# Kernel tuning notes

Measured on AMD Instinct MI355X. Metric: run time of the kernel, lower is better.

The kernel has to match this reference:

```python
import jax, jax.numpy as jnp
import numpy as np

N_NODES = 200000
N_EDGES = 640000
IN_DIM, H1, H2, OUT_DIM = 128, 64, 32, 20


def _glorot(key, shape):
    fan_in, fan_out = shape[0], shape[1]
    lim = float(np.sqrt(6.0 / (fan_in + fan_out)))
    return jax.random.uniform(key, shape, jnp.float32, -lim, lim)


def setup_inputs() -> dict:
    key = jax.random.key(0)
    ks = jax.random.split(key, 8)
    x = jax.random.normal(ks[0], (N_NODES, IN_DIM), jnp.float32)
    edge_index = jax.random.randint(ks[1], (2, N_EDGES), 0, N_NODES, jnp.int64)
    # SAGEConv params: lin_l (neighbor path, with bias), lin_r (root path, no bias)
    return {
        "x": x,
        "edge_index": edge_index,
        "Wl1": _glorot(ks[2], (IN_DIM, H1)), "bl1": jnp.zeros((H1,), jnp.float32),
        "Wr1": _glorot(ks[3], (IN_DIM, H1)),
        "Wl2": _glorot(ks[4], (H1, H2)), "bl2": jnp.zeros((H2,), jnp.float32),
        "Wr2": _glorot(ks[5], (H1, H2)),
        "Wl3": _glorot(ks[6], (H2, OUT_DIM)), "bl3": jnp.zeros((OUT_DIM,), jnp.float32),
        "Wr3": _glorot(ks[7], (H2, OUT_DIM)),
    }


def _sage_conv(x, src, dst, inv_deg, Wl, bl, Wr):
    # mean-aggregate neighbor features: scatter-add x[src] into dst, divide by in-degree
    msgs = x[src]                                            # [E, D] gather
    agg = jax.ops.segment_sum(msgs, dst, num_segments=N_NODES)  # [N, D]
    agg = agg * inv_deg[:, None]                             # mean
    return agg @ Wl + bl + x @ Wr                            # lin_l(agg) + lin_r(x)


def reference(x, edge_index, Wl1, bl1, Wr1, Wl2, bl2, Wr2, Wl3, bl3, Wr3):
    src, dst = edge_index[0], edge_index[1]
    deg = jax.ops.segment_sum(jnp.ones((src.shape[0],), x.dtype), dst,
                              num_segments=N_NODES)
    inv_deg = jnp.where(deg > 0, 1.0 / jnp.maximum(deg, 1.0), 0.0)

    h = jax.nn.relu(_sage_conv(x, src, dst, inv_deg, Wl1, bl1, Wr1))
    # dropout layers are identity in eval mode
    h = jax.nn.relu(_sage_conv(h, src, dst, inv_deg, Wl2, bl2, Wr2))
    return _sage_conv(h, src, dst, inv_deg, Wl3, bl3, Wr3)
```

## Files before the change

### kernel.cpp

```cpp
#include <hip/hip_runtime.h>
#include <hip/hip_bf16.h>


typedef __attribute__((ext_vector_type(8))) short short8;
typedef __attribute__((ext_vector_type(4))) float f32x4;

__device__ inline unsigned short f2b(float x) {
    return __bfloat16_as_ushort(__float2bfloat16(x));
}
__device__ inline float b2f(unsigned short u) {
    return __uint_as_float(((unsigned)u) << 16);
}

__device__ __forceinline__ void gload_lds16(const void* g, void* l) {
    __builtin_amdgcn_global_load_lds(
        (const __attribute__((address_space(1))) void*)g,
        (__attribute__((address_space(3))) void*)l, 16, 0, 0);
}


__global__ void zero_ints(int* __restrict__ p, int n) {
    int i = blockIdx.x * blockDim.x + threadIdx.x;
    if (i < n) p[i] = 0;
}

__global__ void hist_kernel(const int* __restrict__ dst, int* __restrict__ deg, int E) {
    int i = blockIdx.x * blockDim.x + threadIdx.x;
    if (i < E) atomicAdd(&deg[dst[i]], 1);
}

__global__ void scan_reduce(const int* __restrict__ deg, int* __restrict__ bsum, int n) {
    __shared__ int s[256];
    int i = blockIdx.x * 256 + threadIdx.x;
    s[threadIdx.x] = (i < n) ? deg[i] : 0;
    __syncthreads();
    for (int off = 128; off > 0; off >>= 1) {
        if (threadIdx.x < off) s[threadIdx.x] += s[threadIdx.x + off];
        __syncthreads();
    }
    if (threadIdx.x == 0) bsum[blockIdx.x] = s[0];
}

__global__ void scan_top(int* __restrict__ bsum, int nb) {
    __shared__ int s[1024];
    int t = threadIdx.x;
    int v = (t < nb) ? bsum[t] : 0;
    s[t] = v;
    __syncthreads();
    for (int off = 1; off < 1024; off <<= 1) {
        int add = (t >= off) ? s[t - off] : 0;
        __syncthreads();
        s[t] += add;
        __syncthreads();
    }
    if (t < nb) bsum[t] = s[t] - v;
}

__global__ void scan_final(const int* __restrict__ deg, const int* __restrict__ bsum,
                           int* __restrict__ rowptr, int* __restrict__ cursor,
                           int n, int E) {
    __shared__ int s[256];
    int t = threadIdx.x;
    int i = blockIdx.x * 256 + t;
    int v = (i < n) ? deg[i] : 0;
    s[t] = v;
    __syncthreads();
    for (int off = 1; off < 256; off <<= 1) {
        int add = (t >= off) ? s[t - off] : 0;
        __syncthreads();
        s[t] += add;
        __syncthreads();
    }
    int excl = s[t] - v + bsum[blockIdx.x];
    if (i < n) {
        rowptr[i] = excl;
        cursor[i] = excl;
    }
    if (i == 0) rowptr[n] = E;
}

__global__ void fill_kernel(const int* __restrict__ src, const int* __restrict__ dst,
                            int* __restrict__ cursor, int* __restrict__ csr, int E) {
    int e = blockIdx.x * blockDim.x + threadIdx.x;
    if (e < E) {
        int pos = atomicAdd(&cursor[dst[e]], 1);
        csr[pos] = src[e];
    }
}


__launch_bounds__(256, 2)
__global__ void proj1_mfma(const float* __restrict__ x,
                           const float* __restrict__ Wl,
                           const float* __restrict__ Wr,
                           const float* __restrict__ bl,
                           unsigned short* __restrict__ pv,
                           unsigned short* __restrict__ rv,
                           int n) {
    constexpr int S = 4;
    constexpr int TWB = 4;
    constexpr int NCH = TWB * S * 64;

    __shared__ unsigned short sW[NCH * 8];
    __shared__ float sX[2][64 * 128];

    const int b = (int)blockIdx.x;
    const int ch = (b >> 3) & 1;
    const int blk = (b & 7) | ((b >> 4) << 3);
    const int nblk = (int)gridDim.x >> 1;

    const int tid = threadIdx.x;
    for (int chunk = tid; chunk < NCH; chunk += 256) {
        const int lane_c = chunk & 63;
        const int rest = chunk >> 6;
        const int s = rest % S;
        const int t = rest / S;
        const int c = (ch * TWB + t) * 16 + (lane_c & 15);
        const int k0 = s * 32 + (lane_c >> 4) * 8;
        short8 pack;
#pragma unroll
        for (int j = 0; j < 8; ++j) {
            const int k = k0 + j;
            float w = (c < 64) ? Wl[k * 64 + c] : Wr[k * 64 + (c - 64)];
            pack[j] = (short)f2b(w);
        }
        *reinterpret_cast<short8*>(&sW[(size_t)chunk * 8]) = pack;
    }

    const int wave = tid >> 6, lane = tid & 63;
    const int rg = wave;
    const int q = lane >> 4, ln = lane & 15;

    int colg[4];
    float bias[4];
#pragma unroll
    for (int t = 0; t < 4; ++t) {
        colg[t] = ch * 64 + t * 16 + ln;
        bias[t] = (colg[t] >= 64) ? bl[colg[t] - 64] : 0.0f;
    }

    auto stage = [&](int d, int nb) {
#pragma unroll
        for (int i = 0; i < 8; ++i) {
            const int cbase = wave * 512 + i * 64;
            const int ci = cbase + lane;
            const int rl = ci >> 5;
            const int cc = ci & 31;
            int row = nb + rl;
            if (row >= n) row = n - 1;
            const float* g = x + (size_t)row * 128 + (size_t)((cc ^ (rl & 7)) << 2);
            char* l = (char*)&sX[d][0] + (size_t)cbase * 16;
            gload_lds16(g, l);
        }
    };

    auto compute = [&](int d, int nb) {
        const int rowb = nb + rg * 16;
        const int rl = rg * 16 + ln;
        const int swz = rl & 7;
        const float* xbase = &sX[d][(size_t)rl * 128];
        f32x4 acc[4];
#pragma unroll
        for (int t = 0; t < 4; ++t) acc[t] = (f32x4){0.f, 0.f, 0.f, 0.f};
#pragma unroll
        for (int s = 0; s < S; ++s) {
            const int c0 = s * 8 + q * 2;
            float4 v0 = *reinterpret_cast<const float4*>(xbase + ((c0 ^ swz) << 2));
            float4 v1 = *reinterpret_cast<const float4*>(xbase + (((c0 + 1) ^ swz) << 2));
            short8 a;
            a[0] = (short)f2b(v0.x); a[1] = (short)f2b(v0.y);
            a[2] = (short)f2b(v0.z); a[3] = (short)f2b(v0.w);
            a[4] = (short)f2b(v1.x); a[5] = (short)f2b(v1.y);
            a[6] = (short)f2b(v1.z); a[7] = (short)f2b(v1.w);
#pragma unroll
            for (int t = 0; t < 4; ++t) {
                short8 bf = *reinterpret_cast<const short8*>(
                    &sW[((size_t)(t * S + s)) * 512 + (size_t)lane * 8]);
                acc[t] = __builtin_amdgcn_mfma_f32_16x16x32_bf16(a, bf, acc[t], 0, 0, 0);
            }
        }
#pragma unroll
        for (int t = 0; t < 4; ++t) {
            const int c = colg[t];
#pragma unroll
            for (int rr = 0; rr < 4; ++rr) {
                const int row = rowb + q * 4 + rr;
                if (row < n) {
                    if (c < 64)
                        pv[(size_t)row * 64 + c] = f2b(acc[t][rr]);
                    else
                        rv[(size_t)row * 64 + (c - 64)] = f2b(acc[t][rr] + bias[t]);
                }
            }
        }
    };

    constexpr int npi = 64;
    const int stride = nblk * npi;
    int nb = blk * npi;
    if (nb >= n) return;
    stage(0, nb);
    __syncthreads();
    while (true) {
        const int nb1 = nb + stride;
        if (nb1 < n) stage(1, nb1);
        compute(0, nb);
        __syncthreads();
        if (nb1 >= n) break;
        const int nb2 = nb1 + stride;
        if (nb2 < n) stage(0, nb2);
        compute(1, nb1);
        __syncthreads();
        nb = nb2;
        if (nb >= n) break;
    }
}


template <int DIN, int DP, int DR, int DT2, int CH, int NU,
          bool RELU, bool IN_BF16, bool OUT_BF16>
__launch_bounds__(256, 4)
__global__ void proj_mfma(const void* __restrict__ xv,
                          const float* __restrict__ Wl,
                          const float* __restrict__ Wr,
                          const float* __restrict__ bl,
                          void* __restrict__ pv,
                          void* __restrict__ rv,
                          int n) {
    constexpr int WAVES = 4;
    constexpr int TILES = DT2 / 16;
    constexpr int TW = TILES / CH;
    constexpr int S = DIN / 32;
    constexpr int NCH = TW * S * 64;

    __shared__ unsigned short sF[NCH * 8];

    const int ch   = (CH > 1) ? ((int)blockIdx.x % CH) : 0;
    const int blk  = (int)blockIdx.x / CH;
    const int nblk = (int)gridDim.x / CH;

    const int tid = threadIdx.x;
    for (int chunk = tid; chunk < NCH; chunk += 256) {
        const int lane_c = chunk & 63;
        const int rest = chunk >> 6;
        const int s = rest % S;
        const int t = rest / S;
        const int c = (ch * TW + t) * 16 + (lane_c & 15);
        const int k0 = s * 32 + (lane_c >> 4) * 8;
        short8 pack;
#pragma unroll
        for (int j = 0; j < 8; ++j) {
            float w = 0.f;
            const int k = k0 + j;
            if (c < DP) w = Wl[k * DP + c];
            else if (c < DP + DR) w = Wr[k * DR + (c - DP)];
            pack[j] = (short)f2b(w);
        }
        *reinterpret_cast<short8*>(&sF[(size_t)chunk * 8]) = pack;
    }
    __syncthreads();

    const int wave = tid >> 6, lane = tid & 63;
    const int ng = wave;
    const int q = lane >> 4, ln = lane & 15;
    const int colbase = ch * (TW * 16);

    const unsigned short* fbase = &sF[(size_t)lane * 8];

    int colg[TW];
    float bias[TW];
#pragma unroll
    for (int t = 0; t < TW; ++t) {
        colg[t] = colbase + t * 16 + ln;
        bias[t] = (colg[t] >= DP && colg[t] < DP + DR) ? bl[colg[t] - DP] : 0.0f;
    }

    float4 rf0[NU][2 * S], rf1[NU][2 * S];
    short8 rb0[NU][S], rb1[NU][S];

    auto load_groups = [&](float4 (&rf)[NU][2 * S], short8 (&rb)[NU][S], int nbase) {
#pragma unroll
        for (int g = 0; g < NU; ++g) {
            const int base = nbase + (ng * NU + g) * 16;
            if (base >= n) continue;
            if constexpr (IN_BF16) {
                const unsigned short* xr =
                    (const unsigned short*)xv + (size_t)(base + ln) * DIN + q * 8;
#pragma unroll
                for (int s = 0; s < S; ++s)
                    rb[g][s] = *reinterpret_cast<const short8*>(xr + s * 32);
            } else {
                const float* xr = (const float*)xv + (size_t)(base + ln) * DIN + q * 8;
#pragma unroll
                for (int s = 0; s < S; ++s) {
                    rf[g][2 * s]     = *reinterpret_cast<const float4*>(xr + s * 32);
                    rf[g][2 * s + 1] = *reinterpret_cast<const float4*>(xr + s * 32 + 4);
                }
            }
        }
    };

    auto compute_groups = [&](float4 (&rf)[NU][2 * S], short8 (&rb)[NU][S], int nbase) {
#pragma unroll
        for (int g = 0; g < NU; ++g) {
            const int base = nbase + (ng * NU + g) * 16;
            if (base >= n) continue;
            short8 af[S];
#pragma unroll
            for (int s = 0; s < S; ++s) {
                if constexpr (IN_BF16) {
                    short8 a = rb[g][s];
                    if (RELU) {
#pragma unroll
                        for (int j = 0; j < 8; ++j)
                            a[j] = ((short)a[j] < 0) ? (short)0 : a[j];
                    }
                    af[s] = a;
                } else {
                    float4 v0 = rf[g][2 * s], v1 = rf[g][2 * s + 1];
                    if (RELU) {
                        v0.x = fmaxf(v0.x, 0.0f); v0.y = fmaxf(v0.y, 0.0f);
                        v0.z = fmaxf(v0.z, 0.0f); v0.w = fmaxf(v0.w, 0.0f);
                        v1.x = fmaxf(v1.x, 0.0f); v1.y = fmaxf(v1.y, 0.0f);
                        v1.z = fmaxf(v1.z, 0.0f); v1.w = fmaxf(v1.w, 0.0f);
                    }
                    short8 a;
                    a[0] = (short)f2b(v0.x); a[1] = (short)f2b(v0.y);
                    a[2] = (short)f2b(v0.z); a[3] = (short)f2b(v0.w);
                    a[4] = (short)f2b(v1.x); a[5] = (short)f2b(v1.y);
                    a[6] = (short)f2b(v1.z); a[7] = (short)f2b(v1.w);
                    af[s] = a;
                }
            }

            f32x4 acc[TW];
#pragma unroll
            for (int t = 0; t < TW; ++t) acc[t] = (f32x4){0.f, 0.f, 0.f, 0.f};
#pragma unroll
            for (int s = 0; s < S; ++s)
#pragma unroll
                for (int t = 0; t < TW; ++t) {
                    short8 bf = *reinterpret_cast<const short8*>(
                        fbase + (size_t)(t * S + s) * 512);
                    acc[t] = __builtin_amdgcn_mfma_f32_16x16x32_bf16(
                        af[s], bf, acc[t], 0, 0, 0);
                }

#pragma unroll
            for (int t = 0; t < TW; ++t) {
                const int c = colg[t];
#pragma unroll
                for (int rr = 0; rr < 4; ++rr) {
                    const int row = base + q * 4 + rr;
                    if (c < DP) {
                        if constexpr (OUT_BF16)
                            ((unsigned short*)pv)[(size_t)row * DP + c] = f2b(acc[t][rr]);
                        else
                            ((float*)pv)[(size_t)row * DP + c] = acc[t][rr];
                    } else if (c < DP + DR) {
                        const float v = acc[t][rr] + bias[t];
                        if constexpr (OUT_BF16)
                            ((unsigned short*)rv)[(size_t)row * DR + (c - DP)] = f2b(v);
                        else
                            ((float*)rv)[(size_t)row * DR + (c - DP)] = v;
                    }
                }
            }
        }
    };

    const int npi = WAVES * NU * 16;
    const int stride = nblk * npi;
    int nb = blk * npi;
    if (nb >= n) return;
    load_groups(rf0, rb0, nb);
    while (true) {
        const int nb1 = nb + stride;
        if (nb1 < n) load_groups(rf1, rb1, nb1);
        compute_groups(rf0, rb0, nb);
        nb = nb1;
        if (nb >= n) break;
        const int nb2 = nb + stride;
        if (nb2 < n) load_groups(rf0, rb0, nb2);
        compute_groups(rf1, rb1, nb);
        nb = nb2;
        if (nb >= n) break;
    }
}


template <int D, int L>
__global__ void agg_bf16(const int* __restrict__ rowptr,
                         const int* __restrict__ csr,
                         const unsigned short* __restrict__ p,
                         unsigned short* __restrict__ out,
                         int n) {
    constexpr int RQ = D / 8;
    long long gid = (long long)blockIdx.x * blockDim.x + threadIdx.x;
    int d = (int)(gid / L);
    int l = (int)(gid % L);
    if (d >= n) return;
    int beg = rowptr[d], end = rowptr[d + 1];
    int deg = end - beg;
    if (deg <= 0) return;

    const short8* pr = reinterpret_cast<const short8*>(p);
    float s[8];
#pragma unroll
    for (int j = 0; j < 8; ++j) s[j] = 0.0f;

    int i = beg;
    for (; i + 4 <= end; i += 4) {
        int e0 = csr[i], e1 = csr[i + 1], e2 = csr[i + 2], e3 = csr[i + 3];
        short8 a = pr[(size_t)e0 * RQ + l];
        short8 b = pr[(size_t)e1 * RQ + l];
        short8 c = pr[(size_t)e2 * RQ + l];
        short8 e = pr[(size_t)e3 * RQ + l];
#pragma unroll
        for (int j = 0; j < 8; ++j)
            s[j] += (b2f((unsigned short)a[j]) + b2f((unsigned short)b[j])) +
                    (b2f((unsigned short)c[j]) + b2f((unsigned short)e[j]));
    }
    for (; i < end; ++i) {
        short8 a = pr[(size_t)csr[i] * RQ + l];
#pragma unroll
        for (int j = 0; j < 8; ++j) s[j] += b2f((unsigned short)a[j]);
    }

    const float inv = 1.0f / (float)deg;
    short8* o = reinterpret_cast<short8*>(out) + (size_t)d * RQ + l;
    short8 cur = *o;
#pragma unroll
    for (int j = 0; j < 8; ++j) {
        float v = b2f((unsigned short)cur[j]) + s[j] * inv;
        cur[j] = (short)f2b(v);
    }
    *o = cur;
}

template <int D, int L>
__global__ void agg_f32(const int* __restrict__ rowptr,
                        const int* __restrict__ csr,
                        const float* __restrict__ p,
                        float* __restrict__ out,
                        int n) {
    constexpr int RQ = D / 4;
    static_assert(L == RQ, "agg_f32: one float4 per lane");
    long long gid = (long long)blockIdx.x * blockDim.x + threadIdx.x;
    int d = (int)(gid / L);
    int l = (int)(gid % L);
    if (d >= n) return;
    int beg = rowptr[d], end = rowptr[d + 1];
    int deg = end - beg;
    if (deg <= 0) return;

    const float4* pr = reinterpret_cast<const float4*>(p);
    float sx = 0.f, sy = 0.f, sz = 0.f, sw = 0.f;
    int i = beg;
    for (; i + 4 <= end; i += 4) {
        int s0 = csr[i], s1 = csr[i + 1], s2 = csr[i + 2], s3 = csr[i + 3];
        float4 a = pr[(size_t)s0 * RQ + l];
        float4 b = pr[(size_t)s1 * RQ + l];
        float4 c = pr[(size_t)s2 * RQ + l];
        float4 e = pr[(size_t)s3 * RQ + l];
        sx += (a.x + b.x) + (c.x + e.x);
        sy += (a.y + b.y) + (c.y + e.y);
        sz += (a.z + b.z) + (c.z + e.z);
        sw += (a.w + b.w) + (c.w + e.w);
    }
    for (; i < end; ++i) {
        float4 a = pr[(size_t)csr[i] * RQ + l];
        sx += a.x; sy += a.y; sz += a.z; sw += a.w;
    }
    const float inv = 1.0f / (float)deg;
    float4* o = reinterpret_cast<float4*>(out) + (size_t)d * RQ + l;
    float4 cur = *o;
    cur.x += sx * inv; cur.y += sy * inv;
    cur.z += sz * inv; cur.w += sw * inv;
    *o = cur;
}


extern "C" void kernel_launch(void* const* d_in, const int* in_sizes, int n_in,
                              void* d_out, int out_size, void* d_ws, size_t ws_size,
                              hipStream_t stream) {
    const float* x   = (const float*)d_in[0];
    const int*   ei  = (const int*)d_in[1];
    const float* Wl1 = (const float*)d_in[2];
    const float* bl1 = (const float*)d_in[3];
    const float* Wr1 = (const float*)d_in[4];
    const float* Wl2 = (const float*)d_in[5];
    const float* bl2 = (const float*)d_in[6];
    const float* Wr2 = (const float*)d_in[7];
    const float* Wl3 = (const float*)d_in[8];
    const float* bl3 = (const float*)d_in[9];
    const float* Wr3 = (const float*)d_in[10];
    float* out = (float*)d_out;

    const int N = in_sizes[0] / 128;
    const int E = in_sizes[1] / 2;
    const int* src  = ei;
    const int* dstp = ei + E;

    unsigned short* A1 = (unsigned short*)d_ws;
    unsigned short* Bb = A1 + (size_t)N * 64;
    unsigned short* A2 = Bb + (size_t)N * 64;
    unsigned short* Cb = A2 + (size_t)N * 32;
    float* A3 = (float*)(Cb + (size_t)N * 32);
    int* rowptr = (int*)(A3 + (size_t)N * 20);
    int* csr    = rowptr + (N + 1);

    int* degi   = (int*)A3;
    int* cursor = degi + N;
    int* bsum   = cursor + N;

    const int NB = (N + 255) / 256;

    zero_ints<<<NB, 256, 0, stream>>>(degi, N);
    hist_kernel<<<(E + 255) / 256, 256, 0, stream>>>(dstp, degi, E);
    scan_reduce<<<NB, 256, 0, stream>>>(degi, bsum, N);
    scan_top<<<1, 1024, 0, stream>>>(bsum, NB);
    scan_final<<<NB, 256, 0, stream>>>(degi, bsum, rowptr, cursor, N, E);
    fill_kernel<<<(E + 255) / 256, 256, 0, stream>>>(src, dstp, cursor, csr, E);

    proj1_mfma<<<512, 256, 0, stream>>>(x, Wl1, Wr1, bl1, A1, Bb, N);
    agg_bf16<64, 8><<<(int)(((long long)N * 8 + 255) / 256), 256, 0, stream>>>(
        rowptr, csr, A1, Bb, N);

    proj_mfma<64, 32, 32, 64, 1, 2, true, true, true><<<1563, 256, 0, stream>>>(
        Bb, Wl2, Wr2, bl2, A2, Cb, N);
    agg_bf16<32, 4><<<(int)(((long long)N * 4 + 255) / 256), 256, 0, stream>>>(
        rowptr, csr, A2, Cb, N);

    proj_mfma<32, 20, 20, 48, 1, 2, true, true, false><<<1563, 256, 0, stream>>>(
        Cb, Wl3, Wr3, bl3, A3, out, N);
    agg_f32<20, 5><<<(int)(((long long)N * 5 + 255) / 256), 256, 0, stream>>>(
        rowptr, csr, A3, out, N);
}
```

Before: 335.7 us.

## Stage layer-2/3 projection inputs through LDS with async global-to-LDS double buffering

Replaces the register-prefetched proj_mfma for layers 2 and 3 with proj_lds. The new kernel copies 64-row bf16 input tiles into XOR-swizzled shared memory using global_load_lds, double-buffered across grid-stride iterations, before the MFMA reads them. The grid shrinks to 1024 blocks, and the zero-fill kernel becomes hipMemsetAsync. The intent is more coalesced loads and overlap of memory with compute, at the cost of extra barriers and more LDS use per block. The first weight-staging loop has no barrier after it, which relies on the later __syncthreads before compute.

```diff
diff --git a/kernel.cpp b/kernel.cpp
--- a/kernel.cpp
+++ b/kernel.cpp
@@ -18,11 +18,6 @@
         (__attribute__((address_space(3))) void*)l, 16, 0, 0);
 }
 
-
-__global__ void zero_ints(int* __restrict__ p, int n) {
-    int i = blockIdx.x * blockDim.x + threadIdx.x;
-    if (i < n) p[i] = 0;
-}
 
 __global__ void hist_kernel(const int* __restrict__ dst, int* __restrict__ deg, int E) {
     int i = blockIdx.x * blockDim.x + threadIdx.x;
@@ -101,8 +96,8 @@
     constexpr int TWB = 4;
     constexpr int NCH = TWB * S * 64;
 
-    __shared__ unsigned short sW[NCH * 8];
-    __shared__ float sX[2][64 * 128];
+    __shared__ __attribute__((aligned(16))) unsigned short sW[NCH * 8];
+    __shared__ __attribute__((aligned(16))) float sX[2][64 * 128];
 
     const int b = (int)blockIdx.x;
     const int ch = (b >> 3) & 1;
@@ -217,35 +212,33 @@
 }
 
 
-template <int DIN, int DP, int DR, int DT2, int CH, int NU,
-          bool RELU, bool IN_BF16, bool OUT_BF16>
+template <int DIN, int DP, int DR, int DT2, bool RELU, bool OUT_BF16>
 __launch_bounds__(256, 4)
-__global__ void proj_mfma(const void* __restrict__ xv,
-                          const float* __restrict__ Wl,
-                          const float* __restrict__ Wr,
-                          const float* __restrict__ bl,
-                          void* __restrict__ pv,
-                          void* __restrict__ rv,
-                          int n) {
-    constexpr int WAVES = 4;
+__global__ void proj_lds(const unsigned short* __restrict__ xv,
+                         const float* __restrict__ Wl,
+                         const float* __restrict__ Wr,
+                         const float* __restrict__ bl,
+                         void* __restrict__ pv,
+                         void* __restrict__ rv,
+                         int n) {
+    constexpr int S = DIN / 32;
     constexpr int TILES = DT2 / 16;
-    constexpr int TW = TILES / CH;
-    constexpr int S = DIN / 32;
-    constexpr int NCH = TW * S * 64;
-
-    __shared__ unsigned short sF[NCH * 8];
-
-    const int ch   = (CH > 1) ? ((int)blockIdx.x % CH) : 0;
-    const int blk  = (int)blockIdx.x / CH;
-    const int nblk = (int)gridDim.x / CH;
-
+    constexpr int CR = DIN / 8;
+    constexpr int NCH = TILES * S * 64;
+
+    __shared__ __attribute__((aligned(16))) unsigned short sW[NCH * 8];
+    __shared__ __attribute__((aligned(16))) unsigned short sX[2][64 * DIN];
+
+    const int blk = (int)blockIdx.x;
+    const int nblk = (int)gridDim.x;
     const int tid = threadIdx.x;
+
     for (int chunk = tid; chunk < NCH; chunk += 256) {
         const int lane_c = chunk & 63;
         const int rest = chunk >> 6;
         const int s = rest % S;
         const int t = rest / S;
-        const int c = (ch * TW + t) * 16 + (lane_c & 15);
+        const int c = t * 16 + (lane_c & 15);
         const int k0 = s * 32 + (lane_c >> 4) * 8;
         short8 pack;
 #pragma unroll
@@ -256,102 +249,68 @@
             else if (c < DP + DR) w = Wr[k * DR + (c - DP)];
             pack[j] = (short)f2b(w);
         }
-        *reinterpret_cast<short8*>(&sF[(size_t)chunk * 8]) = pack;
-    }
-    __syncthreads();
+        *reinterpret_cast<short8*>(&sW[(size_t)chunk * 8]) = pack;
+    }
 
     const int wave = tid >> 6, lane = tid & 63;
-    const int ng = wave;
+    const int rg = wave;
     const int q = lane >> 4, ln = lane & 15;
-    const int colbase = ch * (TW * 16);
-
-    const unsigned short* fbase = &sF[(size_t)lane * 8];
-
-    int colg[TW];
-    float bias[TW];
-#pragma unroll
-    for (int t = 0; t < TW; ++t) {
-        colg[t] = colbase + t * 16 + ln;
+
+    int colg[TILES];
+    float bias[TILES];
+#pragma unroll
+    for (int t = 0; t < TILES; ++t) {
+        colg[t] = t * 16 + ln;
         bias[t] = (colg[t] >= DP && colg[t] < DP + DR) ? bl[colg[t] - DP] : 0.0f;
     }
 
-    float4 rf0[NU][2 * S], rf1[NU][2 * S];
-    short8 rb0[NU][S], rb1[NU][S];
-
-    auto load_groups = [&](float4 (&rf)[NU][2 * S], short8 (&rb)[NU][S], int nbase) {
-#pragma unroll
-        for (int g = 0; g < NU; ++g) {
-            const int base = nbase + (ng * NU + g) * 16;
-            if (base >= n) continue;
-            if constexpr (IN_BF16) {
-                const unsigned short* xr =
-                    (const unsigned short*)xv + (size_t)(base + ln) * DIN + q * 8;
-#pragma unroll
-                for (int s = 0; s < S; ++s)
-                    rb[g][s] = *reinterpret_cast<const short8*>(xr + s * 32);
-            } else {
-                const float* xr = (const float*)xv + (size_t)(base + ln) * DIN + q * 8;
-#pragma unroll
-                for (int s = 0; s < S; ++s) {
-                    rf[g][2 * s]     = *reinterpret_cast<const float4*>(xr + s * 32);
-                    rf[g][2 * s + 1] = *reinterpret_cast<const float4*>(xr + s * 32 + 4);
-                }
+    auto stage = [&](int d, int nb) {
+#pragma unroll
+        for (int i = 0; i < CR / 4; ++i) {
+            const int cbase = wave * (16 * CR) + i * 64;
+            const int ci = cbase + lane;
+            const int rl = ci / CR;
+            const int cc = ci & (CR - 1);
+            int row = nb + rl;
+            if (row >= n) row = n - 1;
+            const unsigned short* g =
+                xv + (size_t)row * DIN + (size_t)((cc ^ (rl & (CR - 1))) << 3);
+            char* l = (char*)&sX[d][0] + (size_t)cbase * 16;
+            gload_lds16(g, l);
+        }
+    };
+
+    auto compute = [&](int d, int nb) {
+        const int rl = rg * 16 + ln;
+        const int swz = rl & (CR - 1);
+        const unsigned short* rowb = &sX[d][(size_t)rl * DIN];
+        f32x4 acc[TILES];
+#pragma unroll
+        for (int t = 0; t < TILES; ++t) acc[t] = (f32x4){0.f, 0.f, 0.f, 0.f};
+#pragma unroll
+        for (int s = 0; s < S; ++s) {
+            const int c0 = s * 4 + q;
+            short8 a = *reinterpret_cast<const short8*>(rowb + (size_t)((c0 ^ swz) << 3));
+            if (RELU) {
+#pragma unroll
+                for (int j = 0; j < 8; ++j)
+                    a[j] = ((short)a[j] < 0) ? (short)0 : a[j];
             }
-        }
-    };
-
-    auto compute_groups = [&](float4 (&rf)[NU][2 * S], short8 (&rb)[NU][S], int nbase) {
-#pragma unroll
-        for (int g = 0; g < NU; ++g) {
-            const int base = nbase + (ng * NU + g) * 16;
-            if (base >= n) continue;
-            short8 af[S];
-#pragma unroll
-            for (int s = 0; s < S; ++s) {
-                if constexpr (IN_BF16) {
-                    short8 a = rb[g][s];
-                    if (RELU) {
-#pragma unroll
-                        for (int j = 0; j < 8; ++j)
-                            a[j] = ((short)a[j] < 0) ? (short)0 : a[j];
-                    }
-                    af[s] = a;
-                } else {
-                    float4 v0 = rf[g][2 * s], v1 = rf[g][2 * s + 1];
-                    if (RELU) {
-                        v0.x = fmaxf(v0.x, 0.0f); v0.y = fmaxf(v0.y, 0.0f);
-                        v0.z = fmaxf(v0.z, 0.0f); v0.w = fmaxf(v0.w, 0.0f);
-                        v1.x = fmaxf(v1.x, 0.0f); v1.y = fmaxf(v1.y, 0.0f);
-                        v1.z = fmaxf(v1.z, 0.0f); v1.w = fmaxf(v1.w, 0.0f);
-                    }
-                    short8 a;
-                    a[0] = (short)f2b(v0.x); a[1] = (short)f2b(v0.y);
-                    a[2] = (short)f2b(v0.z); a[3] = (short)f2b(v0.w);
-                    a[4] = (short)f2b(v1.x); a[5] = (short)f2b(v1.y);
-                    a[6] = (short)f2b(v1.z); a[7] = (short)f2b(v1.w);
-                    af[s] = a;
-                }
+#pragma unroll
+            for (int t = 0; t < TILES; ++t) {
+                short8 bf = *reinterpret_cast<const short8*>(
+                    &sW[((size_t)(t * S + s)) * 512 + (size_t)lane * 8]);
+                acc[t] = __builtin_amdgcn_mfma_f32_16x16x32_bf16(a, bf, acc[t], 0, 0, 0);
             }
-
-            f32x4 acc[TW];
-#pragma unroll
-            for (int t = 0; t < TW; ++t) acc[t] = (f32x4){0.f, 0.f, 0.f, 0.f};
-#pragma unroll
-            for (int s = 0; s < S; ++s)
-#pragma unroll
-                for (int t = 0; t < TW; ++t) {
-                    short8 bf = *reinterpret_cast<const short8*>(
-                        fbase + (size_t)(t * S + s) * 512);
-                    acc[t] = __builtin_amdgcn_mfma_f32_16x16x32_bf16(
-                        af[s], bf, acc[t], 0, 0, 0);
-                }
-
-#pragma unroll
-            for (int t = 0; t < TW; ++t) {
-                const int c = colg[t];
-#pragma unroll
-                for (int rr = 0; rr < 4; ++rr) {
-                    const int row = base + q * 4 + rr;
+        }
+        const int rowbase = nb + rg * 16 + q * 4;
+#pragma unroll
+        for (int t = 0; t < TILES; ++t) {
+            const int c = colg[t];
+#pragma unroll
+            for (int rr = 0; rr < 4; ++rr) {
+                const int row = rowbase + rr;
+                if (row < n) {
                     if (c < DP) {
                         if constexpr (OUT_BF16)
                             ((unsigned short*)pv)[(size_t)row * DP + c] = f2b(acc[t][rr]);
@@ -369,20 +328,22 @@
         }
     };
 
-    const int npi = WAVES * NU * 16;
+    constexpr int npi = 64;
     const int stride = nblk * npi;
     int nb = blk * npi;
     if (nb >= n) return;
-    load_groups(rf0, rb0, nb);
+    stage(0, nb);
+    __syncthreads();
     while (true) {
         const int nb1 = nb + stride;
-        if (nb1 < n) load_groups(rf1, rb1, nb1);
-        compute_groups(rf0, rb0, nb);
-        nb = nb1;
-        if (nb >= n) break;
-        const int nb2 = nb + stride;
-        if (nb2 < n) load_groups(rf0, rb0, nb2);
-        compute_groups(rf1, rb1, nb);
+        if (nb1 < n) stage(1, nb1);
+        compute(0, nb);
+        __syncthreads();
+        if (nb1 >= n) break;
+        const int nb2 = nb1 + stride;
+        if (nb2 < n) stage(0, nb2);
+        compute(1, nb1);
+        __syncthreads();
         nb = nb2;
         if (nb >= n) break;
     }
@@ -516,7 +477,7 @@
 
     const int NB = (N + 255) / 256;
 
-    zero_ints<<<NB, 256, 0, stream>>>(degi, N);
+    hipMemsetAsync(degi, 0, (size_t)N * sizeof(int), stream);
     hist_kernel<<<(E + 255) / 256, 256, 0, stream>>>(dstp, degi, E);
     scan_reduce<<<NB, 256, 0, stream>>>(degi, bsum, N);
     scan_top<<<1, 1024, 0, stream>>>(bsum, NB);
@@ -527,12 +488,12 @@
     agg_bf16<64, 8><<<(int)(((long long)N * 8 + 255) / 256), 256, 0, stream>>>(
         rowptr, csr, A1, Bb, N);
 
-    proj_mfma<64, 32, 32, 64, 1, 2, true, true, true><<<1563, 256, 0, stream>>>(
+    proj_lds<64, 32, 32, 64, true, true><<<1024, 256, 0, stream>>>(
         Bb, Wl2, Wr2, bl2, A2, Cb, N);
     agg_bf16<32, 4><<<(int)(((long long)N * 4 + 255) / 256), 256, 0, stream>>>(
         rowptr, csr, A2, Cb, N);
 
-    proj_mfma<32, 20, 20, 48, 1, 2, true, true, false><<<1563, 256, 0, stream>>>(
+    proj_lds<32, 20, 20, 48, true, false><<<1024, 256, 0, stream>>>(
         Cb, Wl3, Wr3, bl3, A3, out, N);
     agg_f32<20, 5><<<(int)(((long long)N * 5 + 255) / 256), 256, 0, stream>>>(
         rowptr, csr, A3, out, N);
```

After: 333.2 us. Within noise of the previous version (-0.7%).
